# Performance work log

Measured on AMD Instinct MI355X. Metric: run time of the kernel, lower is better.

Reference implementation:

```python
import jax, jax.numpy as jnp
import numpy as np

NUM_GRAPHS = 64
EPS = 1e-5


def _bn(x, g, b):
    # training-mode BatchNorm1d with biased variance (as torch uses for normalization)
    m = x.mean(axis=0)
    v = x.var(axis=0)
    return (x - m) * jax.lax.rsqrt(v + EPS) * g + b


def setup_inputs() -> dict:
    key = jax.random.key(0)
    ks = jax.random.split(key, 16)
    N, E, F, T, H = 50000, 500000, 8, 8, 64
    d = {
        "x": jax.random.normal(ks[0], (N, F), jnp.float32),
        "edge_index": jax.random.randint(ks[1], (2, E), 0, N),
        "edge_attr": jax.random.uniform(ks[2], (E, T), jnp.float32),
        "batch_index": jnp.sort(jax.random.randint(ks[3], (N,), 0, NUM_GRAPHS)),
        # edge_nn: Linear(T,16) -> ReLU -> Linear(16, F*H)
        "w_e1": jax.random.normal(ks[4], (T, 16), jnp.float32) * 0.2,
        "b_e1": jnp.zeros((16,), jnp.float32),
        "w_e2": jax.random.normal(ks[5], (16, F * H), jnp.float32) * 0.1,
        "b_e2": jnp.zeros((F * H,), jnp.float32),
        # NNConv root weight + bias
        "root": jax.random.normal(ks[6], (F, H), jnp.float32) * 0.2,
        "conv_bias": jnp.zeros((H,), jnp.float32),
        "g_bnc": jnp.ones((H,), jnp.float32), "b_bnc": jnp.zeros((H,), jnp.float32),
        "w1": jax.random.normal(ks[7], (2 * H, 256), jnp.float32) * 0.08,
        "b1": jnp.zeros((256,), jnp.float32),
        "g1": jnp.ones((256,), jnp.float32), "be1": jnp.zeros((256,), jnp.float32),
        "w2": jax.random.normal(ks[8], (256, 128), jnp.float32) * 0.08,
        "b2": jnp.zeros((128,), jnp.float32),
        "g2": jnp.ones((128,), jnp.float32), "be2": jnp.zeros((128,), jnp.float32),
        "w3": jax.random.normal(ks[9], (128, 64), jnp.float32) * 0.1,
        "b3": jnp.zeros((64,), jnp.float32),
        "g3": jnp.ones((64,), jnp.float32), "be3": jnp.zeros((64,), jnp.float32),
        "wout": jax.random.normal(ks[10], (64, 10), jnp.float32) * 0.1,
        "bout": jnp.zeros((10,), jnp.float32),
    }
    return d


def reference(x, edge_index, edge_attr, batch_index,
              w_e1, b_e1, w_e2, b_e2, root, conv_bias, g_bnc, b_bnc,
              w1, b1, g1, be1, w2, b2, g2, be2, w3, b3, g3, be3, wout, bout):
    N, F = x.shape
    H = root.shape[1]
    src, dst = edge_index[0], edge_index[1]

    # edge-conditioned weights: edge_nn(edge_attr) -> [E, F, H]
    h_e = jax.nn.relu(edge_attr @ w_e1 + b_e1)
    W_e = (h_e @ w_e2 + b_e2).reshape(-1, F, H)

    # gather source features, per-edge matmul, scatter-mean into targets
    msg = jnp.einsum('ef,efh->eh', x[src], W_e)            # [E, H]
    agg = jax.ops.segment_sum(msg, dst, num_segments=N)
    deg = jax.ops.segment_sum(jnp.ones((msg.shape[0],), msg.dtype), dst, num_segments=N)
    agg = agg / jnp.maximum(deg, 1.0)[:, None]
    h = x @ root + agg + conv_bias                          # NNConv output [N, H]

    h = jax.nn.relu(_bn(h, g_bnc, b_bnc))

    # global mean + max pooling per graph
    gs = jax.ops.segment_sum(h, batch_index, num_segments=NUM_GRAPHS)
    cnt = jax.ops.segment_sum(jnp.ones((N,), h.dtype), batch_index, num_segments=NUM_GRAPHS)
    gmean = gs / jnp.maximum(cnt, 1.0)[:, None]
    gmax = jax.ops.segment_max(h, batch_index, num_segments=NUM_GRAPHS)
    gmax = jnp.where(cnt[:, None] > 0, gmax, 0.0)
    g = jnp.concatenate([gmean, gmax], axis=1)              # [G, 2H]

    g = jax.nn.relu(_bn(g @ w1 + b1, g1, be1))
    g = jax.nn.relu(_bn(g @ w2 + b2, g2, be2))
    g = jax.nn.relu(_bn(g @ w3 + b3, g3, be3))
    return g @ wout + bout
```

## Files before the change

kernel.cpp:

```cpp
#include <hip/hip_runtime.h>

#define DEG_CAP 64
#define ZROW 136

__device__ __forceinline__ int rfl(int v) { return __builtin_amdgcn_readfirstlane(v); }

__global__ void k_he(const float* __restrict__ ea, const float* __restrict__ w,
                     const float* __restrict__ b, float* __restrict__ he, int E) {
  int e = blockIdx.x * blockDim.x + threadIdx.x;
  if (e >= E) return;
  const float4* eap = reinterpret_cast<const float4*>(ea + (size_t)e * 8);
  float4 a0 = eap[0], a1 = eap[1];
  float av[8] = {a0.x, a0.y, a0.z, a0.w, a1.x, a1.y, a1.z, a1.w};
  float o[16];
#pragma unroll
  for (int k = 0; k < 16; ++k) o[k] = b[k];
#pragma unroll
  for (int t = 0; t < 8; ++t) {
    float at = av[t];
#pragma unroll
    for (int k = 0; k < 16; ++k) o[k] = fmaf(at, w[t * 16 + k], o[k]);
  }
#pragma unroll
  for (int k = 0; k < 16; ++k) o[k] = fmaxf(o[k], 0.f);
  float4* hp = reinterpret_cast<float4*>(he + (size_t)e * 16);
  hp[0] = make_float4(o[0], o[1], o[2], o[3]);
  hp[1] = make_float4(o[4], o[5], o[6], o[7]);
  hp[2] = make_float4(o[8], o[9], o[10], o[11]);
  hp[3] = make_float4(o[12], o[13], o[14], o[15]);
}

__global__ void k_fill(const int* __restrict__ ei, int* __restrict__ cursor,
                       int* __restrict__ slots, int E) {
  int e = blockIdx.x * blockDim.x + threadIdx.x;
  if (e >= E) return;
  int dst = ei[E + e];
  int slot = atomicAdd(&cursor[dst], 1);
  if (slot < DEG_CAP) slots[(size_t)dst * DEG_CAP + slot] = e;
}

__global__ void k_zgather(const float* __restrict__ x, const int* __restrict__ ei,
                          const float* __restrict__ he, const int* __restrict__ cursor,
                          const int* __restrict__ slots, float* __restrict__ zbuf,
                          int N) {
  int lane = threadIdx.x & 63;
  int n = rfl(blockIdx.x * (blockDim.x >> 6) + (threadIdx.x >> 6));
  if (n >= N) return;
  int k = lane >> 2;
  int f2 = (lane & 3) << 1;
  int d = cursor[n];
  int dc = min(d, DEG_CAP);
  int eid = (lane < dc) ? slots[(size_t)n * DEG_CAP + lane] : 0;
  int sid = ei[eid];
  float z0 = 0.f, z1 = 0.f, xs0 = 0.f, xs1 = 0.f;
  if (dc > 0) {
    int e0 = __shfl(eid, 0), s0 = __shfl(sid, 0);
    float hk = he[(size_t)e0 * 16 + k];
    float2 xv = *reinterpret_cast<const float2*>(x + (size_t)s0 * 8 + f2);
    for (int i = 1; i < dc; ++i) {
      int e1 = __shfl(eid, i), s1 = __shfl(sid, i);
      float hk_n = he[(size_t)e1 * 16 + k];
      float2 xv_n = *reinterpret_cast<const float2*>(x + (size_t)s1 * 8 + f2);
      z0 = fmaf(hk, xv.x, z0);
      z1 = fmaf(hk, xv.y, z1);
      xs0 += xv.x; xs1 += xv.y;
      hk = hk_n; xv = xv_n;
    }
    z0 = fmaf(hk, xv.x, z0);
    z1 = fmaf(hk, xv.y, z1);
    xs0 += xv.x; xs1 += xv.y;
  }
  float2* zp = reinterpret_cast<float2*>(zbuf + (size_t)n * ZROW);
  zp[lane] = make_float2(z0, z1);
  if (lane < 4) zp[64 + lane] = make_float2(xs0, xs1);
}

__global__ __launch_bounds__(256, 2) void k_wmix(
    const float* __restrict__ x, const int* __restrict__ cursor,
    const float* __restrict__ zbuf, const float* __restrict__ w_e2,
    const float* __restrict__ b_e2, const float* __restrict__ root,
    const float* __restrict__ conv_bias, float* __restrict__ hout,
    float* __restrict__ stats, int N) {
  int lane = threadIdx.x & 63;
  int wid = rfl(blockIdx.x * (blockDim.x >> 6) + (threadIdx.x >> 6));
  int nw = gridDim.x * (blockDim.x >> 6);

  float w2r[128];
#pragma unroll
  for (int j = 0; j < 128; ++j) {
    int k = j >> 3;
    int f = (((j >> 1) & 3) << 1) + (j & 1);
    w2r[j] = w_e2[k * 512 + f * 64 + lane];
  }
  float b2r[8], rootr[8];
#pragma unroll
  for (int f = 0; f < 8; ++f) b2r[f] = b_e2[f * 64 + lane];
#pragma unroll
  for (int f = 0; f < 8; ++f) rootr[f] = root[f * 64 + lane];
  float cb = conv_bias[lane];

  float bnsum = 0.f, bnsq = 0.f;
  for (int n = wid; n < N; n += nw) {
    const float* zr = zbuf + (size_t)n * ZROW;
    float agg = 0.f;
#pragma unroll
    for (int j = 0; j < 128; ++j) agg = fmaf(zr[j], w2r[j], agg);
    float xb = 0.f;
#pragma unroll
    for (int f = 0; f < 8; ++f) xb = fmaf(zr[128 + f], b2r[f], xb);
    int d = cursor[n];
    float hval = cb + (agg + xb) / (float)max(d, 1);
    const float* xn = x + (size_t)n * 8;
#pragma unroll
    for (int f = 0; f < 8; ++f) hval = fmaf(xn[f], rootr[f], hval);
    hout[(size_t)n * 64 + lane] = hval;
    bnsum += hval;
    bnsq += hval * hval;
  }
  atomicAdd(&stats[lane], bnsum);
  atomicAdd(&stats[64 + lane], bnsq);
}

__global__ void k_bnpool(const float* __restrict__ hbuf, const float* __restrict__ stats,
                         const int* __restrict__ batch, const float* __restrict__ gamma,
                         const float* __restrict__ beta, float* __restrict__ gsum,
                         unsigned int* __restrict__ gmax, int* __restrict__ gcnt, int N) {
  int lane = threadIdx.x & 63;
  int wid = blockIdx.x * (blockDim.x >> 6) + (threadIdx.x >> 6);
  int nw = gridDim.x * (blockDim.x >> 6);
  float m = stats[lane] / (float)N;
  float var = stats[64 + lane] / (float)N - m * m;
  float rs = rsqrtf(var + 1e-5f);
  float ga = gamma[lane], be = beta[lane];
  int per = (N + nw - 1) / nw;
  int n0 = wid * per;
  int n1 = min(N, n0 + per);
  int cur = -1, cnt = 0;
  float s = 0.f, mx = 0.f;
  for (int n = n0; n < n1; ++n) {
    int g = batch[n];
    float v = hbuf[(size_t)n * 64 + lane];
    float y = fmaxf(fmaf((v - m) * rs, ga, be), 0.f);
    if (g != cur) {
      if (cur >= 0) {
        atomicAdd(&gsum[cur * 64 + lane], s);
        atomicMax(&gmax[cur * 64 + lane], __float_as_uint(mx));
        if (lane == 0) atomicAdd(&gcnt[cur], cnt);
      }
      cur = g; s = 0.f; mx = 0.f; cnt = 0;
    }
    s += y; mx = fmaxf(mx, y); ++cnt;
  }
  if (cur >= 0) {
    atomicAdd(&gsum[cur * 64 + lane], s);
    atomicMax(&gmax[cur * 64 + lane], __float_as_uint(mx));
    if (lane == 0) atomicAdd(&gcnt[cur], cnt);
  }
}

__global__ void k_head_pool(const float* __restrict__ gsum,
                            const unsigned int* __restrict__ gmax,
                            const int* __restrict__ gcnt,
                            const float* __restrict__ W, const float* __restrict__ b,
                            const float* __restrict__ gamma, const float* __restrict__ beta,
                            float* __restrict__ out, int Kout) {
  int lane = threadIdx.x & 63;
  int col = blockIdx.x * (blockDim.x >> 6) + (threadIdx.x >> 6);
  if (col >= Kout) return;
  float inv = 1.f / fmaxf((float)gcnt[lane], 1.f);
  float a = b[col];
#pragma unroll 4
  for (int k = 0; k < 64; ++k)
    a = fmaf(gsum[lane * 64 + k] * inv, W[(size_t)k * Kout + col], a);
#pragma unroll 4
  for (int k = 0; k < 64; ++k)
    a = fmaf(__uint_as_float(gmax[lane * 64 + k]), W[(size_t)(64 + k) * Kout + col], a);
  float sv = a, ss = a * a;
#pragma unroll
  for (int off = 32; off > 0; off >>= 1) {
    sv += __shfl_xor(sv, off);
    ss += __shfl_xor(ss, off);
  }
  float m = sv * (1.f / 64.f);
  float var = ss * (1.f / 64.f) - m * m;
  float y = fmaxf(fmaf((a - m) * rsqrtf(var + 1e-5f), gamma[col], beta[col]), 0.f);
  out[(size_t)lane * Kout + col] = y;
}

__global__ void k_head(const float* __restrict__ in, const float* __restrict__ W,
                       const float* __restrict__ b, const float* __restrict__ gamma,
                       const float* __restrict__ beta, float* __restrict__ out,
                       int Kin, int Kout) {
  int lane = threadIdx.x & 63;
  int col = blockIdx.x * (blockDim.x >> 6) + (threadIdx.x >> 6);
  if (col >= Kout) return;
  const float4* ir = reinterpret_cast<const float4*>(in + (size_t)lane * Kin);
  float a = b[col];
  for (int k4 = 0; k4 < (Kin >> 2); ++k4) {
    float4 v = ir[k4];
    int k = k4 << 2;
    a = fmaf(v.x, W[(size_t)k * Kout + col], a);
    a = fmaf(v.y, W[(size_t)(k + 1) * Kout + col], a);
    a = fmaf(v.z, W[(size_t)(k + 2) * Kout + col], a);
    a = fmaf(v.w, W[(size_t)(k + 3) * Kout + col], a);
  }
  float sv = a, ss = a * a;
#pragma unroll
  for (int off = 32; off > 0; off >>= 1) {
    sv += __shfl_xor(sv, off);
    ss += __shfl_xor(ss, off);
  }
  float m = sv * (1.f / 64.f);
  float var = ss * (1.f / 64.f) - m * m;
  float y = fmaxf(fmaf((a - m) * rsqrtf(var + 1e-5f), gamma[col], beta[col]), 0.f);
  out[(size_t)lane * Kout + col] = y;
}

__global__ void k_out(const float* __restrict__ in, const float* __restrict__ W,
                      const float* __restrict__ b, float* __restrict__ out) {
  int t = threadIdx.x;
  if (t >= 640) return;
  int r = t / 10, c = t % 10;
  float a = b[c];
#pragma unroll
  for (int k = 0; k < 64; ++k) a = fmaf(in[r * 64 + k], W[k * 10 + c], a);
  out[t] = a;
}

extern "C" void kernel_launch(void* const* d_in, const int* in_sizes, int n_in,
                              void* d_out, int out_size, void* d_ws, size_t ws_size,
                              hipStream_t stream) {
  const float* x = (const float*)d_in[0];
  const int* ei = (const int*)d_in[1];
  const float* ea = (const float*)d_in[2];
  const int* batch = (const int*)d_in[3];
  const float* w_e1 = (const float*)d_in[4];
  const float* b_e1 = (const float*)d_in[5];
  const float* w_e2 = (const float*)d_in[6];
  const float* b_e2 = (const float*)d_in[7];
  const float* root = (const float*)d_in[8];
  const float* conv_bias = (const float*)d_in[9];
  const float* g_bnc = (const float*)d_in[10];
  const float* b_bnc = (const float*)d_in[11];
  const float* w1 = (const float*)d_in[12];
  const float* b1 = (const float*)d_in[13];
  const float* g1 = (const float*)d_in[14];
  const float* be1 = (const float*)d_in[15];
  const float* w2 = (const float*)d_in[16];
  const float* b2 = (const float*)d_in[17];
  const float* g2 = (const float*)d_in[18];
  const float* be2 = (const float*)d_in[19];
  const float* w3 = (const float*)d_in[20];
  const float* b3 = (const float*)d_in[21];
  const float* g3 = (const float*)d_in[22];
  const float* be3 = (const float*)d_in[23];
  const float* wout = (const float*)d_in[24];
  const float* bout = (const float*)d_in[25];

  int N = in_sizes[0] / 8;
  int E = in_sizes[1] / 2;

  char* wsb = (char*)d_ws;
  size_t off = 0;
  auto alloc = [&](size_t bytes) -> void* {
    void* p = wsb + off;
    off += (bytes + 255) & ~(size_t)255;
    return p;
  };
  float* he = (float*)alloc((size_t)E * 16 * 4);
  int* cursor = (int*)alloc((size_t)N * 4);
  int* slots = (int*)alloc((size_t)N * DEG_CAP * 4);
  float* zbuf = (float*)alloc((size_t)N * ZROW * 4);
  float* hbuf = (float*)alloc((size_t)N * 64 * 4);
  float* zblk = (float*)alloc(8384 * 4);
  float* stats = zblk;
  float* gsum = zblk + 128;
  unsigned int* gmax = (unsigned int*)(zblk + 128 + 4096);
  int* gcnt = (int*)(zblk + 128 + 8192);
  float* l1 = (float*)alloc(64 * 256 * 4);
  float* l2 = (float*)alloc(64 * 128 * 4);
  float* l3 = (float*)alloc(64 * 64 * 4);

  hipMemsetAsync(cursor, 0, (size_t)N * 4, stream);
  hipMemsetAsync(zblk, 0, 8384 * 4, stream);

  const int tb = 256;
  k_he<<<(E + tb - 1) / tb, tb, 0, stream>>>(ea, w_e1, b_e1, he, E);
  k_fill<<<(E + tb - 1) / tb, tb, 0, stream>>>(ei, cursor, slots, E);
  k_zgather<<<(N + 3) / 4, 256, 0, stream>>>(x, ei, he, cursor, slots, zbuf, N);
  k_wmix<<<768, 256, 0, stream>>>(x, cursor, zbuf, w_e2, b_e2, root, conv_bias,
                                  hbuf, stats, N);
  k_bnpool<<<512, 256, 0, stream>>>(hbuf, stats, batch, g_bnc, b_bnc, gsum, gmax, gcnt, N);
  k_head_pool<<<64, 256, 0, stream>>>(gsum, gmax, gcnt, w1, b1, g1, be1, l1, 256);
  k_head<<<32, 256, 0, stream>>>(l1, w2, b2, g2, be2, l2, 256, 128);
  k_head<<<16, 256, 0, stream>>>(l2, w3, b3, g3, be3, l3, 128, 64);
  k_out<<<1, 640, 0, stream>>>(l3, wout, bout, (float*)d_out);
}
```

Measured before the change: 368.4 us.

## Replace per-node wave mixing kernel with LDS-tiled 64-node GEMM over augmented z rows

The gather kernel now pre-divides by degree and appends the node's raw features to each z row, so the whole NNConv output becomes one GEMM of [N,144] by [144,64]. The new kernel tiles 64 nodes per block, stages both the weights and the z tile in LDS, and computes a 4x4 register tile per thread. BN statistics are reduced through shuffles and LDS before a single global atomic per block. This replaces the old kernel, which read each z row from global memory with per-lane scalar loads and held 128 weights in registers per lane. The cost is that every block reloads the full weight matrix into LDS, and the z rows grow larger.

```diff
diff --git a/kernel.cpp b/kernel.cpp
--- a/kernel.cpp
+++ b/kernel.cpp
@@ -1,7 +1,8 @@
 #include <hip/hip_runtime.h>
 
 #define DEG_CAP 64
-#define ZROW 136
+#define ZROW 144
+#define ZPAD 148
 
 __device__ __forceinline__ int rfl(int v) { return __builtin_amdgcn_readfirstlane(v); }
 
@@ -70,55 +71,109 @@
     z1 = fmaf(hk, xv.y, z1);
     xs0 += xv.x; xs1 += xv.y;
   }
+  float inv = 1.f / (float)max(d, 1);
+  z0 *= inv; z1 *= inv; xs0 *= inv; xs1 *= inv;
   float2* zp = reinterpret_cast<float2*>(zbuf + (size_t)n * ZROW);
   zp[lane] = make_float2(z0, z1);
   if (lane < 4) zp[64 + lane] = make_float2(xs0, xs1);
-}
-
-__global__ __launch_bounds__(256, 2) void k_wmix(
-    const float* __restrict__ x, const int* __restrict__ cursor,
+  if (lane < 8) zbuf[(size_t)n * ZROW + 136 + lane] = x[(size_t)n * 8 + lane];
+}
+
+__global__ __launch_bounds__(256) void k_zwgemm(
     const float* __restrict__ zbuf, const float* __restrict__ w_e2,
     const float* __restrict__ b_e2, const float* __restrict__ root,
     const float* __restrict__ conv_bias, float* __restrict__ hout,
     float* __restrict__ stats, int N) {
-  int lane = threadIdx.x & 63;
-  int wid = rfl(blockIdx.x * (blockDim.x >> 6) + (threadIdx.x >> 6));
-  int nw = gridDim.x * (blockDim.x >> 6);
-
-  float w2r[128];
-#pragma unroll
-  for (int j = 0; j < 128; ++j) {
-    int k = j >> 3;
-    int f = (((j >> 1) & 3) << 1) + (j & 1);
-    w2r[j] = w_e2[k * 512 + f * 64 + lane];
-  }
-  float b2r[8], rootr[8];
-#pragma unroll
-  for (int f = 0; f < 8; ++f) b2r[f] = b_e2[f * 64 + lane];
-#pragma unroll
-  for (int f = 0; f < 8; ++f) rootr[f] = root[f * 64 + lane];
-  float cb = conv_bias[lane];
-
-  float bnsum = 0.f, bnsq = 0.f;
-  for (int n = wid; n < N; n += nw) {
-    const float* zr = zbuf + (size_t)n * ZROW;
-    float agg = 0.f;
-#pragma unroll
-    for (int j = 0; j < 128; ++j) agg = fmaf(zr[j], w2r[j], agg);
-    float xb = 0.f;
-#pragma unroll
-    for (int f = 0; f < 8; ++f) xb = fmaf(zr[128 + f], b2r[f], xb);
-    int d = cursor[n];
-    float hval = cb + (agg + xb) / (float)max(d, 1);
-    const float* xn = x + (size_t)n * 8;
-#pragma unroll
-    for (int f = 0; f < 8; ++f) hval = fmaf(xn[f], rootr[f], hval);
-    hout[(size_t)n * 64 + lane] = hval;
-    bnsum += hval;
-    bnsq += hval * hval;
-  }
-  atomicAdd(&stats[lane], bnsum);
-  atomicAdd(&stats[64 + lane], bnsq);
+  __shared__ float wt[ZROW * 64];
+  __shared__ float zt[64 * ZPAD];
+  __shared__ float sl[128];
+  int t = threadIdx.x;
+  int n0 = blockIdx.x * 64;
+
+  for (int i = t; i < ZROW * 64; i += 256) {
+    int j = i >> 6, hh = i & 63;
+    float v;
+    if (j < 128) {
+      int k = j >> 3, f = (((j >> 1) & 3) << 1) | (j & 1);
+      v = w_e2[k * 512 + f * 64 + hh];
+    } else if (j < 136) {
+      v = b_e2[(j - 128) * 64 + hh];
+    } else {
+      v = root[(j - 136) * 64 + hh];
+    }
+    wt[i] = v;
+  }
+  for (int i4 = t; i4 < 64 * ZROW / 4; i4 += 256) {
+    int dw = i4 << 2;
+    int r = dw / ZROW;
+    int c = dw - r * ZROW;
+    float4 v = make_float4(0.f, 0.f, 0.f, 0.f);
+    if (n0 + r < N)
+      v = *reinterpret_cast<const float4*>(zbuf + (size_t)(n0 + r) * ZROW + c);
+    *reinterpret_cast<float4*>(&zt[r * ZPAD + c]) = v;
+  }
+  if (t < 128) sl[t] = 0.f;
+  __syncthreads();
+
+  int hg = t & 15;
+  int ng = t >> 4;
+  float acc[4][4];
+#pragma unroll
+  for (int i = 0; i < 4; ++i)
+#pragma unroll
+    for (int q = 0; q < 4; ++q) acc[i][q] = 0.f;
+
+  for (int j = 0; j < ZROW; j += 4) {
+    float za[4][4], wa[4][4];
+#pragma unroll
+    for (int i = 0; i < 4; ++i) {
+      float4 v = *reinterpret_cast<const float4*>(&zt[(ng * 4 + i) * ZPAD + j]);
+      za[i][0] = v.x; za[i][1] = v.y; za[i][2] = v.z; za[i][3] = v.w;
+    }
+#pragma unroll
+    for (int r = 0; r < 4; ++r) {
+      float4 v = *reinterpret_cast<const float4*>(&wt[(j + r) * 64 + hg * 4]);
+      wa[r][0] = v.x; wa[r][1] = v.y; wa[r][2] = v.z; wa[r][3] = v.w;
+    }
+#pragma unroll
+    for (int r = 0; r < 4; ++r)
+#pragma unroll
+      for (int i = 0; i < 4; ++i)
+#pragma unroll
+        for (int q = 0; q < 4; ++q)
+          acc[i][q] = fmaf(za[i][r], wa[r][q], acc[i][q]);
+  }
+
+  float cb[4];
+#pragma unroll
+  for (int q = 0; q < 4; ++q) cb[q] = conv_bias[hg * 4 + q];
+  float bns[4] = {0.f, 0.f, 0.f, 0.f}, bnq[4] = {0.f, 0.f, 0.f, 0.f};
+#pragma unroll
+  for (int i = 0; i < 4; ++i) {
+    int n = n0 + ng * 4 + i;
+    float h0 = acc[i][0] + cb[0], h1 = acc[i][1] + cb[1];
+    float h2 = acc[i][2] + cb[2], h3 = acc[i][3] + cb[3];
+    if (n < N) {
+      *reinterpret_cast<float4*>(&hout[(size_t)n * 64 + hg * 4]) =
+          make_float4(h0, h1, h2, h3);
+      bns[0] += h0; bns[1] += h1; bns[2] += h2; bns[3] += h3;
+      bnq[0] += h0 * h0; bnq[1] += h1 * h1; bnq[2] += h2 * h2; bnq[3] += h3 * h3;
+    }
+  }
+#pragma unroll
+  for (int q = 0; q < 4; ++q) {
+    bns[q] += __shfl_xor(bns[q], 16); bns[q] += __shfl_xor(bns[q], 32);
+    bnq[q] += __shfl_xor(bnq[q], 16); bnq[q] += __shfl_xor(bnq[q], 32);
+  }
+  if ((t & 48) == 0) {
+#pragma unroll
+    for (int q = 0; q < 4; ++q) {
+      atomicAdd(&sl[hg * 4 + q], bns[q]);
+      atomicAdd(&sl[64 + hg * 4 + q], bnq[q]);
+    }
+  }
+  __syncthreads();
+  if (t < 128) atomicAdd(&stats[t], sl[t]);
 }
 
 __global__ void k_bnpool(const float* __restrict__ hbuf, const float* __restrict__ stats,
@@ -288,8 +343,8 @@
   k_he<<<(E + tb - 1) / tb, tb, 0, stream>>>(ea, w_e1, b_e1, he, E);
   k_fill<<<(E + tb - 1) / tb, tb, 0, stream>>>(ei, cursor, slots, E);
   k_zgather<<<(N + 3) / 4, 256, 0, stream>>>(x, ei, he, cursor, slots, zbuf, N);
-  k_wmix<<<768, 256, 0, stream>>>(x, cursor, zbuf, w_e2, b_e2, root, conv_bias,
-                                  hbuf, stats, N);
+  k_zwgemm<<<(N + 63) / 64, 256, 0, stream>>>(zbuf, w_e2, b_e2, root, conv_bias,
+                                              hbuf, stats, N);
   k_bnpool<<<512, 256, 0, stream>>>(hbuf, stats, batch, g_bnc, b_bnc, gsum, gmax, gcnt, N);
   k_head_pool<<<64, 256, 0, stream>>>(gsum, gmax, gcnt, w1, b1, g1, be1, l1, 256);
   k_head<<<32, 256, 0, stream>>>(l1, w2, b2, g2, be2, l2, 256, 128);
```

New measurement: 308.7 us. 1.19x faster.
